# Optimization experiments

Hardware: AMD Instinct MI355X
Metric: run time of the kernel (lower is better)

## Reference

```python
import jax, jax.numpy as jnp
import numpy as np

N_HEAD = 16
MA_K = 0.02          # sigmoid temperature in ma_k_activation
LEAKY_SLOPE = 0.02   # negative_slope in ma_q_activation
NEG_INF = -1e9


def setup_inputs() -> dict:
    key = jax.random.key(0)
    k1, k2, k3, k4 = jax.random.split(key, 4)
    B, T, C = 2, 2048, 1024
    x = jax.random.normal(k1, (B, T, C), dtype=jnp.float32)
    s = 1.0 / np.sqrt(C)
    W_attn = jax.random.normal(k2, (C, 2 * C), dtype=jnp.float32) * s
    W_k2 = jax.random.normal(k3, (C, C), dtype=jnp.float32) * s
    W_proj = jax.random.normal(k4, (C, C), dtype=jnp.float32) * s
    return {"x": x, "W_attn": W_attn, "W_k2": W_k2, "W_proj": W_proj}


def _heads(t, H):
    # [B,T,C] -> [B,H,T,d]
    B, T, C = t.shape
    return t.reshape(B, T, H, C // H).transpose(0, 2, 1, 3)


def reference(x, W_attn, W_k2, W_proj):
    B, T, C = x.shape
    H = N_HEAD
    d = C // H
    scale = 1.0 / jnp.sqrt(jnp.asarray(d, x.dtype))

    qk = x @ W_attn                      # [B,T,2C]
    q, k = jnp.split(qk, 2, axis=-1)
    q = _heads(q, H)                     # [B,H,T,d]
    k = _heads(k, H)
    v = _heads(x, H)                     # v = x

    # --- AR branch: causal softmax attention ---
    scores = jnp.einsum('bhtd,bhsd->bhts', q, k) * scale
    causal = jnp.tril(jnp.ones((T, T), dtype=bool))
    scores = jnp.where(causal, scores, NEG_INF)
    attn = jax.nn.softmax(scores, axis=-1)
    y = jnp.einsum('bhts,bhsd->bhtd', attn, v)   # [B,H,T,d]

    # --- MA branch: causal, softmax-free linear attention on residual ---
    e = v[:, :, 1:, :] - y[:, :, :-1, :]          # [B,H,T-1,d]
    k2 = _heads(x[:, :-1, :] @ W_k2, H)           # [B,H,T-1,d]
    q2 = q[:, :, 1:, :]                           # [B,H,T-1,d]

    qa = -jax.nn.leaky_relu(-q2 * scale, negative_slope=LEAKY_SLOPE)
    ka = jax.nn.sigmoid(MA_K * (k2 * scale))

    w = jnp.einsum('bhtd,bhsd->bhts', qa, ka)     # [B,H,T-1,T-1]
    w = jnp.tril(w)
    y2 = jnp.einsum('bhts,bhsd->bhtd', w, e)      # [B,H,T-1,d]
    y2 = jnp.concatenate([jnp.zeros_like(y2[:, :, :1, :]), y2], axis=2)  # pad front

    def merge(t):  # [B,H,T,d] -> [B,T,C]
        return t.transpose(0, 2, 1, 3).reshape(B, T, C)

    return merge(y) @ W_proj + merge(y2) @ W_proj
```

## Files before the change

### kernel.cpp

```cpp
#include <hip/hip_runtime.h>

typedef unsigned short u16;
typedef u16   u16x4  __attribute__((ext_vector_type(4)));
typedef u16   u16x8  __attribute__((ext_vector_type(8)));
typedef __bf16 bf16x8 __attribute__((ext_vector_type(8)));
typedef float  f32x4  __attribute__((ext_vector_type(4)));

__device__ __forceinline__ float bf2f(u16 v) {
    unsigned u = ((unsigned)v) << 16;
    return __builtin_bit_cast(float, u);
}
__device__ __forceinline__ u16 f2bf(float f) {
    unsigned u = __builtin_bit_cast(unsigned, f);
    u += 0x7fffu + ((u >> 16) & 1u);
    return (u16)(u >> 16);
}

__device__ __forceinline__ size_t kimg_idx(int bh, int s, int d) {
    return ((size_t)(bh * 32 + (s >> 6)) * 4096) + (size_t)(((d >> 3) * 64 + (s & 63)) * 8) + (d & 7);
}
__device__ __forceinline__ size_t vimg_idx(int bh, int s, int d) {
    return ((size_t)(bh * 32 + (s >> 6)) * 4096) + (size_t)((((s & 63) >> 3) * 64 + d) * 8) + (s & 7);
}

__global__ __launch_bounds__(256)
void convert_pack(const float* __restrict__ in, u16* __restrict__ xb,
                  u16* __restrict__ xpack) {
    int i = blockIdx.x * 256 + threadIdx.x;
    int c4 = i & 255, row = i >> 8;
    int s = row & 2047, b = row >> 11;
    float4 v = ((const float4*)in)[i];
    u16x4 o;
    o.x = f2bf(v.x); o.y = f2bf(v.y); o.z = f2bf(v.z); o.w = f2bf(v.w);
    ((u16x4*)xb)[i] = o;
    int h = c4 >> 4, d0 = (c4 & 15) * 4;
    size_t base = vimg_idx(b * 16 + h, s, d0);
    xpack[base]      = o.x;
    xpack[base + 8]  = o.y;
    xpack[base + 16] = o.z;
    xpack[base + 24] = o.w;
}

__global__ __launch_bounds__(256)
void prep_weights(const float* __restrict__ Wa, const float* __restrict__ Wk,
                  const float* __restrict__ Wp, u16* __restrict__ Wta,
                  u16* __restrict__ Wtk, u16* __restrict__ Wtp) {
    __shared__ u16 tile[64][65];
    const int bx = blockIdx.x;
    const float* in; u16* out; int Cd, cx;
    if (bx < 32)      { in = Wa; out = Wta; Cd = 2048; cx = bx; }
    else if (bx < 48) { in = Wk; out = Wtk; Cd = 1024; cx = bx - 32; }
    else              { in = Wp; out = Wtp; Cd = 1024; cx = bx - 48; }
    const int c0 = cx * 64, r0 = blockIdx.y * 64;
    const int tid = threadIdx.x;
#pragma unroll
    for (int i = 0; i < 16; ++i) {
        int idx = tid + i * 256;
        int r = idx >> 6, c = idx & 63;
        tile[r][c] = f2bf(in[(size_t)(r0 + r) * Cd + c0 + c]);
    }
    __syncthreads();
#pragma unroll
    for (int i = 0; i < 16; ++i) {
        int idx = tid + i * 256;
        int r = idx >> 6, c = idx & 63;
        out[(size_t)(c0 + r) * 1024 + r0 + c] = tile[c][r];
    }
}

__global__ __launch_bounds__(256, 3)
void gemm_fused(const u16* __restrict__ A, const u16* __restrict__ Bt,
                u16* __restrict__ qs, u16* __restrict__ kpack,
                u16* __restrict__ kapack) {
    const int K = 1024;
    __shared__ __align__(16) u16 As[4][128][8];
    __shared__ __align__(16) u16 Bs[4][128][8];
    const int tid = threadIdx.x;
    const int wave = tid >> 6, lane = tid & 63;
    const int m0 = blockIdx.y * 128, n0 = blockIdx.x * 128;
    const int wm = (wave >> 1) * 64, wn = (wave & 1) * 64;
    const int q = lane >> 4, mr = lane & 15;
    const int sr = tid >> 2, c8 = tid & 3;
    const int sw = c8 * 2;
    const int rs = q * 2;
    const u16* Ap = A + (size_t)(m0 + sr) * K + c8 * 8;
    const u16* Bp = Bt + (size_t)(n0 + sr) * K + c8 * 8;

    f32x4 acc[4][4];
#pragma unroll
    for (int i = 0; i < 4; ++i)
#pragma unroll
        for (int j = 0; j < 4; ++j) acc[i][j] = f32x4{0.f, 0.f, 0.f, 0.f};

    u16x8 a0, a1, b0, b1;
    auto gload = [&](int k0) {
        a0 = *(const u16x8*)(Ap + k0);
        a1 = *(const u16x8*)(Ap + k0 + (size_t)64 * K);
        b0 = *(const u16x8*)(Bp + k0);
        b1 = *(const u16x8*)(Bp + k0 + (size_t)64 * K);
    };
    gload(0);
    for (int k0 = 0; k0 < K; k0 += 32) {
        __syncthreads();
        *(u16x8*)&As[c8][sr ^ sw][0]        = a0;
        *(u16x8*)&As[c8][(sr + 64) ^ sw][0] = a1;
        *(u16x8*)&Bs[c8][sr ^ sw][0]        = b0;
        *(u16x8*)&Bs[c8][(sr + 64) ^ sw][0] = b1;
        __syncthreads();
        if (k0 + 32 < K) gload(k0 + 32);
        bf16x8 af[4], bfr[4];
#pragma unroll
        for (int i = 0; i < 4; ++i) af[i]  = *(const bf16x8*)&As[q][(wm + i * 16 + mr) ^ rs][0];
#pragma unroll
        for (int j = 0; j < 4; ++j) bfr[j] = *(const bf16x8*)&Bs[q][(wn + j * 16 + mr) ^ rs][0];
#pragma unroll
        for (int i = 0; i < 4; ++i)
#pragma unroll
            for (int j = 0; j < 4; ++j)
                acc[i][j] = __builtin_amdgcn_mfma_f32_16x16x32_bf16(af[i], bfr[j], acc[i][j], 0, 0, 0);
    }
#pragma unroll
    for (int i = 0; i < 4; ++i)
#pragma unroll
        for (int j = 0; j < 4; ++j)
#pragma unroll
            for (int r = 0; r < 4; ++r) {
                int m = m0 + wm + i * 16 + q * 4 + r;
                int n = n0 + wn + j * 16 + mr;
                float v = acc[i][j][r];
                int b = m >> 11, s = m & 2047;
                if (n < 1024) {
                    qs[(size_t)m * 1024 + n] = f2bf(v * 0.125f);
                } else if (n < 2048) {
                    int nn = n - 1024;
                    kpack[kimg_idx(b * 16 + (nn >> 6), s, nn & 63)] = f2bf(v);
                } else {
                    int nn = n - 2048;
                    kapack[kimg_idx(b * 16 + (nn >> 6), s, nn & 63)] =
                        f2bf(1.f / (1.f + __expf(-0.0025f * v)));
                }
            }
}

__global__ __launch_bounds__(256, 2)
void gemm64(const u16* __restrict__ A, const u16* __restrict__ Bt,
            float* __restrict__ Cv, int N, int K) {
    __shared__ __align__(16) u16 As[4][64][8];
    __shared__ __align__(16) u16 Bs[4][128][8];
    const int tid = threadIdx.x;
    const int wave = tid >> 6, lane = tid & 63;
    const int m0 = blockIdx.y * 64, n0 = blockIdx.x * 128;
    const int wn0 = wave * 32;
    const int q = lane >> 4, mr = lane & 15;
    const int sr = tid >> 2, c8 = tid & 3;
    const int sw = c8 * 2, rs = q * 2;
    const u16* Ap = A + (size_t)(m0 + sr) * K + c8 * 8;
    const u16* Bp = Bt + (size_t)(n0 + sr) * K + c8 * 8;

    f32x4 acc[4][2];
#pragma unroll
    for (int i = 0; i < 4; ++i)
#pragma unroll
        for (int j = 0; j < 2; ++j) acc[i][j] = f32x4{0.f, 0.f, 0.f, 0.f};

    u16x8 a0, b0, b1;
    auto gload = [&](int k0) {
        a0 = *(const u16x8*)(Ap + k0);
        b0 = *(const u16x8*)(Bp + k0);
        b1 = *(const u16x8*)(Bp + k0 + (size_t)64 * K);
    };
    gload(0);
    for (int k0 = 0; k0 < K; k0 += 32) {
        __syncthreads();
        if (sr < 64) *(u16x8*)&As[c8][sr ^ sw][0] = a0;
        else         *(u16x8*)&As[c8][(sr - 64) ^ sw][0] = a0;
        *(u16x8*)&Bs[c8][sr ^ sw][0]        = b0;
        *(u16x8*)&Bs[c8][(sr + 64) ^ sw][0] = b1;
        __syncthreads();
        if (k0 + 32 < K) gload(k0 + 32);
        bf16x8 af[4], bfr[2];
#pragma unroll
        for (int i = 0; i < 4; ++i) af[i]  = *(const bf16x8*)&As[q][(i * 16 + mr) ^ rs][0];
#pragma unroll
        for (int j = 0; j < 2; ++j) bfr[j] = *(const bf16x8*)&Bs[q][(wn0 + j * 16 + mr) ^ rs][0];
#pragma unroll
        for (int i = 0; i < 4; ++i)
#pragma unroll
            for (int j = 0; j < 2; ++j)
                acc[i][j] = __builtin_amdgcn_mfma_f32_16x16x32_bf16(af[i], bfr[j], acc[i][j], 0, 0, 0);
    }
#pragma unroll
    for (int i = 0; i < 4; ++i)
#pragma unroll
        for (int j = 0; j < 2; ++j)
#pragma unroll
            for (int r = 0; r < 4; ++r) {
                int m = m0 + i * 16 + q * 4 + r;
                int n = n0 + wn0 + j * 16 + mr;
                Cv[(size_t)m * N + n] = acc[i][j][r];
            }
}

__global__ __launch_bounds__(256, 2)
void flash_mfma(const u16* __restrict__ qs, const u16* __restrict__ kpack,
                const u16* __restrict__ xpack, u16* __restrict__ Opart,
                float* __restrict__ lpart) {
    __shared__ __align__(16) u16 Ks[8][64][8];
    __shared__ __align__(16) u16 Vs[8][64][8];
    __shared__ __align__(16) u16 Ps[4][16][72];
    const int bh = blockIdx.y, b = bh >> 4, hc = (bh & 15) * 64;
    const int z = blockIdx.z;
    const int tid = threadIdx.x, w = tid >> 6, lane = tid & 63;
    const int n16 = lane & 15, quad = lane >> 4;
    const u16* kbase = kpack + (size_t)bh * 32 * 4096;
    const u16* vbase = xpack + (size_t)bh * 32 * 4096;
    u16* Ob = Opart + (size_t)z * 4096 * 1024;
    float* lb = lpart + z * 65536;

    for (int rep = 0; rep < 2; ++rep) {
        const int T = rep ? 15 - (int)blockIdx.x : (int)blockIdx.x;
        const int t0 = T * 128;
        const int nchunk = 2 * T + 2;

        bf16x8 qf[2][2];
#pragma unroll
        for (int mt = 0; mt < 2; ++mt) {
            const int trow = t0 + (w + mt * 4) * 16 + n16;
            const u16* qp = &qs[(size_t)(b * 2048 + trow) * 1024 + hc + quad * 8];
            qf[mt][0] = *(const bf16x8*)qp;
            qf[mt][1] = *(const bf16x8*)(qp + 32);
        }

        f32x4 O[2][4];
        float lsum[2][4];
#pragma unroll
        for (int mt = 0; mt < 2; ++mt)
#pragma unroll
            for (int jt = 0; jt < 4; ++jt) { O[mt][jt] = f32x4{0.f, 0.f, 0.f, 0.f}; }
#pragma unroll
        for (int mt = 0; mt < 2; ++mt)
#pragma unroll
            for (int r = 0; r < 4; ++r) lsum[mt][r] = 0.f;

        u16x8 kr0, kr1, vr0, vr1;
        auto pref = [&](int c) {
            const u16* kc = kbase + (size_t)c * 4096;
            const u16* vc = vbase + (size_t)c * 4096;
            kr0 = *(const u16x8*)(kc + tid * 8);
            kr1 = *(const u16x8*)(kc + (256 + tid) * 8);
            vr0 = *(const u16x8*)(vc + tid * 8);
            vr1 = *(const u16x8*)(vc + (256 + tid) * 8);
        };
        if (z < nchunk) pref(z);

        for (int c = z; c < nchunk; c += 2) {
            __syncthreads();
            *(u16x8*)((u16*)Ks + tid * 8)         = kr0;
            *(u16x8*)((u16*)Ks + (256 + tid) * 8) = kr1;
            *(u16x8*)((u16*)Vs + tid * 8)         = vr0;
            *(u16x8*)((u16*)Vs + (256 + tid) * 8) = vr1;
            __syncthreads();
            if (c + 2 < nchunk) pref(c + 2);

            f32x4 S[2][4];
#pragma unroll
            for (int mt = 0; mt < 2; ++mt)
#pragma unroll
                for (int jt = 0; jt < 4; ++jt) S[mt][jt] = f32x4{0.f, 0.f, 0.f, 0.f};
#pragma unroll
            for (int ks = 0; ks < 2; ++ks)
#pragma unroll
                for (int jt = 0; jt < 4; ++jt) {
                    bf16x8 kf = *(const bf16x8*)&Ks[ks * 4 + quad][jt * 16 + n16][0];
                    S[0][jt] = __builtin_amdgcn_mfma_f32_16x16x32_bf16(qf[0][ks], kf, S[0][jt], 0, 0, 0);
                    S[1][jt] = __builtin_amdgcn_mfma_f32_16x16x32_bf16(qf[1][ks], kf, S[1][jt], 0, 0, 0);
                }
            bf16x8 vf[2][4];
#pragma unroll
            for (int ks = 0; ks < 2; ++ks)
#pragma unroll
                for (int jt = 0; jt < 4; ++jt)
                    vf[ks][jt] = *(const bf16x8*)&Vs[ks * 4 + quad][jt * 16 + n16][0];

#pragma unroll
            for (int mt = 0; mt < 2; ++mt) {
                if (mt == 0 && c == 2 * T + 1) continue;
                float p[4][4];
#pragma unroll
                for (int reg = 0; reg < 4; ++reg)
#pragma unroll
                    for (int jt = 0; jt < 4; ++jt)
                        p[reg][jt] = __expf(S[mt][jt][reg]);
                if (c == 2 * T + mt) {
#pragma unroll
                    for (int reg = 0; reg < 4; ++reg) {
                        const int tr = t0 + (w + mt * 4) * 16 + quad * 4 + reg;
#pragma unroll
                        for (int jt = 0; jt < 4; ++jt)
                            if (c * 64 + jt * 16 + n16 > tr) p[reg][jt] = 0.f;
                    }
                }
#pragma unroll
                for (int reg = 0; reg < 4; ++reg) {
                    lsum[mt][reg] += (p[reg][0] + p[reg][1]) + (p[reg][2] + p[reg][3]);
#pragma unroll
                    for (int jt = 0; jt < 4; ++jt)
                        Ps[w][quad * 4 + reg][jt * 16 + n16] = f2bf(p[reg][jt]);
                }
                bf16x8 pf[2];
#pragma unroll
                for (int ks = 0; ks < 2; ++ks)
                    pf[ks] = *(const bf16x8*)&Ps[w][n16][ks * 32 + quad * 8];
#pragma unroll
                for (int ks = 0; ks < 2; ++ks)
#pragma unroll
                    for (int jt = 0; jt < 4; ++jt)
                        O[mt][jt] = __builtin_amdgcn_mfma_f32_16x16x32_bf16(pf[ks], vf[ks][jt], O[mt][jt], 0, 0, 0);
            }
        }

#pragma unroll
        for (int mt = 0; mt < 2; ++mt)
#pragma unroll
            for (int reg = 0; reg < 4; ++reg) {
                float l = lsum[mt][reg];
#pragma unroll
                for (int off = 1; off < 16; off <<= 1) l += __shfl_xor(l, off, 64);
                const int tr = t0 + (w + mt * 4) * 16 + quad * 4 + reg;
                if (n16 == 0) lb[bh * 2048 + tr] = l;
                const size_t row = (size_t)(b * 2048 + tr) * 1024 + hc;
#pragma unroll
                for (int jt = 0; jt < 4; ++jt)
                    Ob[row + jt * 16 + n16] = f2bf(O[mt][jt][reg]);
            }
    }
}

__global__ __launch_bounds__(256)
void combine_flash(const u16* __restrict__ Opart, const float* __restrict__ lpart,
                   const u16* __restrict__ xb, u16* __restrict__ y,
                   u16* __restrict__ epack) {
    int i = blockIdx.x * 256 + threadIdx.x;
    int c4 = i & 255, row = i >> 8, t = row & 2047, b = row >> 11;
    int h = c4 >> 4, d0 = (c4 & 15) * 4;
    size_t off = (size_t)row * 1024 + c4 * 4;
    u16x4 o0 = *(const u16x4*)&Opart[off];
    u16x4 o1 = *(const u16x4*)&Opart[(size_t)4096 * 1024 + off];
    int lrow = (b * 16 + h) * 2048 + t;
    float inv = 1.f / (lpart[lrow] + lpart[65536 + lrow]);
    float y0 = (bf2f(o0.x) + bf2f(o1.x)) * inv;
    float y1 = (bf2f(o0.y) + bf2f(o1.y)) * inv;
    float y2 = (bf2f(o0.z) + bf2f(o1.z)) * inv;
    float y3 = (bf2f(o0.w) + bf2f(o1.w)) * inv;
    u16x4 yo;
    yo.x = f2bf(y0); yo.y = f2bf(y1); yo.z = f2bf(y2); yo.w = f2bf(y3);
    *(u16x4*)&y[off] = yo;
    float e0 = 0.f, e1 = 0.f, e2 = 0.f, e3 = 0.f;
    if (t < 2047) {
        u16x4 xv = *(const u16x4*)&xb[off + 1024];
        e0 = bf2f(xv.x) - y0; e1 = bf2f(xv.y) - y1;
        e2 = bf2f(xv.z) - y2; e3 = bf2f(xv.w) - y3;
    }
    size_t base = vimg_idx(b * 16 + h, t, d0);
    epack[base]      = f2bf(e0);
    epack[base + 8]  = f2bf(e1);
    epack[base + 16] = f2bf(e2);
    epack[base + 24] = f2bf(e3);
}

__global__ __launch_bounds__(256, 2)
void arma_mfma(const u16* __restrict__ qs, const u16* __restrict__ kapack,
               const u16* __restrict__ epack, u16* __restrict__ Opart) {
    __shared__ __align__(16) u16 Ks[8][64][8];
    __shared__ __align__(16) u16 Es[8][64][8];
    __shared__ __align__(16) u16 Ps[4][16][72];
    const int bh = blockIdx.y, b = bh >> 4, hc = (bh & 15) * 64;
    const int z = blockIdx.z;
    const int tid = threadIdx.x, w = tid >> 6, lane = tid & 63;
    const int n16 = lane & 15, quad = lane >> 4;
    const u16* kbase = kapack + (size_t)bh * 32 * 4096;
    const u16* vbase = epack + (size_t)bh * 32 * 4096;
    u16* Ob = Opart + (size_t)z * 4096 * 1024;

    for (int rep = 0; rep < 2; ++rep) {
        const int T = rep ? 15 - (int)blockIdx.x : (int)blockIdx.x;
        const int t0 = T * 128;
        const int nchunk = 2 * T + 2;

        bf16x8 qf[2][2];
#pragma unroll
        for (int mt = 0; mt < 2; ++mt) {
            const int trow = t0 + (w + mt * 4) * 16 + n16;
            const u16* qp = &qs[(size_t)(b * 2048 + trow) * 1024 + hc + quad * 8];
#pragma unroll
            for (int ks = 0; ks < 2; ++ks) {
                u16x8 qv = *(const u16x8*)(qp + ks * 32);
                u16x8 o;
#pragma unroll
                for (int j = 0; j < 8; ++j) {
                    float zv = bf2f(qv[j]);
                    o[j] = f2bf(zv < 0.f ? zv : 0.02f * zv);
                }
                qf[mt][ks] = __builtin_bit_cast(bf16x8, o);
            }
        }

        f32x4 O[2][4];
#pragma unroll
        for (int mt = 0; mt < 2; ++mt)
#pragma unroll
            for (int jt = 0; jt < 4; ++jt) O[mt][jt] = f32x4{0.f, 0.f, 0.f, 0.f};

        u16x8 kr0, kr1, vr0, vr1;
        auto pref = [&](int c) {
            const u16* kc = kbase + (size_t)c * 4096;
            const u16* vc = vbase + (size_t)c * 4096;
            kr0 = *(const u16x8*)(kc + tid * 8);
            kr1 = *(const u16x8*)(kc + (256 + tid) * 8);
            vr0 = *(const u16x8*)(vc + tid * 8);
            vr1 = *(const u16x8*)(vc + (256 + tid) * 8);
        };
        if (z < nchunk) pref(z);

        for (int c = z; c < nchunk; c += 2) {
            __syncthreads();
            *(u16x8*)((u16*)Ks + tid * 8)         = kr0;
            *(u16x8*)((u16*)Ks + (256 + tid) * 8) = kr1;
            *(u16x8*)((u16*)Es + tid * 8)         = vr0;
            *(u16x8*)((u16*)Es + (256 + tid) * 8) = vr1;
            __syncthreads();
            if (c + 2 < nchunk) pref(c + 2);

            f32x4 S[2][4];
#pragma unroll
            for (int mt = 0; mt < 2; ++mt)
#pragma unroll
                for (int jt = 0; jt < 4; ++jt) S[mt][jt] = f32x4{0.f, 0.f, 0.f, 0.f};
#pragma unroll
            for (int ks = 0; ks < 2; ++ks)
#pragma unroll
                for (int jt = 0; jt < 4; ++jt) {
                    bf16x8 kf = *(const bf16x8*)&Ks[ks * 4 + quad][jt * 16 + n16][0];
                    S[0][jt] = __builtin_amdgcn_mfma_f32_16x16x32_bf16(qf[0][ks], kf, S[0][jt], 0, 0, 0);
                    S[1][jt] = __builtin_amdgcn_mfma_f32_16x16x32_bf16(qf[1][ks], kf, S[1][jt], 0, 0, 0);
                }
            bf16x8 vf[2][4];
#pragma unroll
            for (int ks = 0; ks < 2; ++ks)
#pragma unroll
                for (int jt = 0; jt < 4; ++jt)
                    vf[ks][jt] = *(const bf16x8*)&Es[ks * 4 + quad][jt * 16 + n16][0];

#pragma unroll
            for (int mt = 0; mt < 2; ++mt) {
                if (mt == 0 && c == 2 * T + 1) continue;
                if (c == 2 * T + mt) {
#pragma unroll
                    for (int reg = 0; reg < 4; ++reg) {
                        const int tr = t0 + (w + mt * 4) * 16 + quad * 4 + reg;
#pragma unroll
                        for (int jt = 0; jt < 4; ++jt)
                            if (c * 64 + jt * 16 + n16 >= tr) S[mt][jt][reg] = 0.f;
                    }
                }
#pragma unroll
                for (int reg = 0; reg < 4; ++reg)
#pragma unroll
                    for (int jt = 0; jt < 4; ++jt)
                        Ps[w][quad * 4 + reg][jt * 16 + n16] = f2bf(S[mt][jt][reg]);
                bf16x8 pf[2];
#pragma unroll
                for (int ks = 0; ks < 2; ++ks)
                    pf[ks] = *(const bf16x8*)&Ps[w][n16][ks * 32 + quad * 8];
#pragma unroll
                for (int ks = 0; ks < 2; ++ks)
#pragma unroll
                    for (int jt = 0; jt < 4; ++jt)
                        O[mt][jt] = __builtin_amdgcn_mfma_f32_16x16x32_bf16(pf[ks], vf[ks][jt], O[mt][jt], 0, 0, 0);
            }
        }

#pragma unroll
        for (int mt = 0; mt < 2; ++mt)
#pragma unroll
            for (int reg = 0; reg < 4; ++reg) {
                const int tr = t0 + (w + mt * 4) * 16 + quad * 4 + reg;
                const size_t row = (size_t)(b * 2048 + tr) * 1024 + hc;
#pragma unroll
                for (int jt = 0; jt < 4; ++jt)
                    Ob[row + jt * 16 + n16] = f2bf(O[mt][jt][reg]);
            }
    }
}

__global__ __launch_bounds__(256)
void combine_arma(const u16* __restrict__ Opart, const u16* __restrict__ y,
                  u16* __restrict__ ys) {
    int i = blockIdx.x * 256 + threadIdx.x;
    size_t off = (size_t)i * 4;
    u16x4 o0 = *(const u16x4*)&Opart[off];
    u16x4 o1 = *(const u16x4*)&Opart[(size_t)4096 * 1024 + off];
    u16x4 yv = *(const u16x4*)&y[off];
    u16x4 r;
    r.x = f2bf(bf2f(yv.x) + bf2f(o0.x) + bf2f(o1.x));
    r.y = f2bf(bf2f(yv.y) + bf2f(o0.y) + bf2f(o1.y));
    r.z = f2bf(bf2f(yv.z) + bf2f(o0.z) + bf2f(o1.z));
    r.w = f2bf(bf2f(yv.w) + bf2f(o0.w) + bf2f(o1.w));
    *(u16x4*)&ys[off] = r;
}

extern "C" void kernel_launch(void* const* d_in, const int* in_sizes, int n_in,
                              void* d_out, int out_size, void* d_ws, size_t ws_size,
                              hipStream_t stream) {
    const float* x      = (const float*)d_in[0];
    const float* W_attn = (const float*)d_in[1];
    const float* W_k2   = (const float*)d_in[2];
    const float* W_proj = (const float*)d_in[3];
    float* out = (float*)d_out;

    char* w = (char*)d_ws;
    u16* xb      = (u16*)w; w += (size_t)4096 * 1024 * 2;
    u16* Wt_attn = (u16*)w; w += (size_t)2048 * 1024 * 2;
    u16* Wt_k2   = (u16*)w; w += (size_t)1024 * 1024 * 2;
    u16* Wt_proj = (u16*)w; w += (size_t)1024 * 1024 * 2;
    u16* qs      = (u16*)w; w += (size_t)4096 * 1024 * 2;
    u16* kpack   = (u16*)w; w += (size_t)4096 * 1024 * 2;
    u16* kapack  = (u16*)w; w += (size_t)4096 * 1024 * 2;
    u16* xpack   = (u16*)w; w += (size_t)4096 * 1024 * 2;
    u16* y       = (u16*)w; w += (size_t)4096 * 1024 * 2;
    u16* epack   = (u16*)w; w += (size_t)4096 * 1024 * 2;
    u16* Opart   = (u16*)w; w += (size_t)2 * 4096 * 1024 * 2;
    float* lpart = (float*)w; w += (size_t)2 * 65536 * 4;
    u16* ys = xb;

    convert_pack<<<dim3(4096), dim3(256), 0, stream>>>(x, xb, xpack);
    prep_weights<<<dim3(64, 16), dim3(256), 0, stream>>>(W_attn, W_k2, W_proj,
                                                         Wt_attn, Wt_k2, Wt_proj);
    gemm_fused<<<dim3(24, 32), dim3(256), 0, stream>>>(xb, Wt_attn, qs, kpack, kapack);
    flash_mfma<<<dim3(8, 32, 2), dim3(256), 0, stream>>>(qs, kpack, xpack, Opart, lpart);
    combine_flash<<<dim3(4096), dim3(256), 0, stream>>>(Opart, lpart, xb, y, epack);
    arma_mfma<<<dim3(8, 32, 2), dim3(256), 0, stream>>>(qs, kapack, epack, Opart);
    combine_arma<<<dim3(4096), dim3(256), 0, stream>>>(Opart, y, ys);
    gemm64<<<dim3(8, 64), dim3(256), 0, stream>>>(ys, Wt_proj, out, 1024, 1024);
}
```

Baseline: 260.8 us.

## Stage GEMM tiles via direct global-to-LDS async loads instead of register staging

Both GEMM kernels now copy A/B tiles straight into shared memory with global_load_lds 16-byte transfers, replacing the register-staged software prefetch and the XOR swizzle. This cuts VGPR use and the separate LDS store instructions. In exchange, the next tile is no longer prefetched during compute: each iteration waits on vmcnt(0) before the barrier, which exposes global load latency. The unswizzled LDS layout may also bring back bank conflicts on the fragment reads.

Result: slower. 296.6 us (+13.7%).

```diff
diff --git a/kernel.cpp b/kernel.cpp
--- a/kernel.cpp
+++ b/kernel.cpp
@@ -14,6 +14,13 @@
     unsigned u = __builtin_bit_cast(unsigned, f);
     u += 0x7fffu + ((u >> 16) & 1u);
     return (u16)(u >> 16);
+}
+
+__device__ __forceinline__ void async16(const u16* g, u16* l) {
+    __builtin_amdgcn_global_load_lds(
+        (const __attribute__((address_space(1))) unsigned int*)g,
+        (__attribute__((address_space(3))) unsigned int*)l,
+        16, 0, 0);
 }
 
 __device__ __forceinline__ size_t kimg_idx(int bh, int s, int d) {
@@ -80,11 +87,16 @@
     const int m0 = blockIdx.y * 128, n0 = blockIdx.x * 128;
     const int wm = (wave >> 1) * 64, wn = (wave & 1) * 64;
     const int q = lane >> 4, mr = lane & 15;
-    const int sr = tid >> 2, c8 = tid & 3;
-    const int sw = c8 * 2;
-    const int rs = q * 2;
-    const u16* Ap = A + (size_t)(m0 + sr) * K + c8 * 8;
-    const u16* Bp = Bt + (size_t)(n0 + sr) * K + c8 * 8;
+
+    const int s0 = tid, s1 = 256 + tid;
+    const u16* gA0 = A  + (size_t)(m0 + (s0 & 127)) * K + (s0 >> 7) * 8;
+    const u16* gA1 = A  + (size_t)(m0 + (s1 & 127)) * K + (s1 >> 7) * 8;
+    const u16* gB0 = Bt + (size_t)(n0 + (s0 & 127)) * K + (s0 >> 7) * 8;
+    const u16* gB1 = Bt + (size_t)(n0 + (s1 & 127)) * K + (s1 >> 7) * 8;
+    u16* lA0 = &As[0][0][0] + (size_t)s0 * 8;
+    u16* lA1 = &As[0][0][0] + (size_t)s1 * 8;
+    u16* lB0 = &Bs[0][0][0] + (size_t)s0 * 8;
+    u16* lB1 = &Bs[0][0][0] + (size_t)s1 * 8;
 
     f32x4 acc[4][4];
 #pragma unroll
@@ -92,27 +104,19 @@
 #pragma unroll
         for (int j = 0; j < 4; ++j) acc[i][j] = f32x4{0.f, 0.f, 0.f, 0.f};
 
-    u16x8 a0, a1, b0, b1;
-    auto gload = [&](int k0) {
-        a0 = *(const u16x8*)(Ap + k0);
-        a1 = *(const u16x8*)(Ap + k0 + (size_t)64 * K);
-        b0 = *(const u16x8*)(Bp + k0);
-        b1 = *(const u16x8*)(Bp + k0 + (size_t)64 * K);
-    };
-    gload(0);
     for (int k0 = 0; k0 < K; k0 += 32) {
         __syncthreads();
-        *(u16x8*)&As[c8][sr ^ sw][0]        = a0;
-        *(u16x8*)&As[c8][(sr + 64) ^ sw][0] = a1;
-        *(u16x8*)&Bs[c8][sr ^ sw][0]        = b0;
-        *(u16x8*)&Bs[c8][(sr + 64) ^ sw][0] = b1;
+        async16(gA0 + k0, lA0);
+        async16(gA1 + k0, lA1);
+        async16(gB0 + k0, lB0);
+        async16(gB1 + k0, lB1);
+        asm volatile("s_waitcnt vmcnt(0)" ::: "memory");
         __syncthreads();
-        if (k0 + 32 < K) gload(k0 + 32);
         bf16x8 af[4], bfr[4];
 #pragma unroll
-        for (int i = 0; i < 4; ++i) af[i]  = *(const bf16x8*)&As[q][(wm + i * 16 + mr) ^ rs][0];
-#pragma unroll
-        for (int j = 0; j < 4; ++j) bfr[j] = *(const bf16x8*)&Bs[q][(wn + j * 16 + mr) ^ rs][0];
+        for (int i = 0; i < 4; ++i) af[i]  = *(const bf16x8*)&As[q][wm + i * 16 + mr][0];
+#pragma unroll
+        for (int j = 0; j < 4; ++j) bfr[j] = *(const bf16x8*)&Bs[q][wn + j * 16 + mr][0];
 #pragma unroll
         for (int i = 0; i < 4; ++i)
 #pragma unroll
@@ -152,10 +156,14 @@
     const int m0 = blockIdx.y * 64, n0 = blockIdx.x * 128;
     const int wn0 = wave * 32;
     const int q = lane >> 4, mr = lane & 15;
-    const int sr = tid >> 2, c8 = tid & 3;
-    const int sw = c8 * 2, rs = q * 2;
-    const u16* Ap = A + (size_t)(m0 + sr) * K + c8 * 8;
-    const u16* Bp = Bt + (size_t)(n0 + sr) * K + c8 * 8;
+
+    const u16* gA = A + (size_t)(m0 + (tid & 63)) * K + (tid >> 6) * 8;
+    u16* lA = &As[0][0][0] + (size_t)tid * 8;
+    const int s1 = 256 + tid;
+    const u16* gB0 = Bt + (size_t)(n0 + (tid & 127)) * K + (tid >> 7) * 8;
+    const u16* gB1 = Bt + (size_t)(n0 + (s1 & 127)) * K + (s1 >> 7) * 8;
+    u16* lB0 = &Bs[0][0][0] + (size_t)tid * 8;
+    u16* lB1 = &Bs[0][0][0] + (size_t)s1 * 8;
 
     f32x4 acc[4][2];
 #pragma unroll
@@ -163,26 +171,18 @@
 #pragma unroll
         for (int j = 0; j < 2; ++j) acc[i][j] = f32x4{0.f, 0.f, 0.f, 0.f};
 
-    u16x8 a0, b0, b1;
-    auto gload = [&](int k0) {
-        a0 = *(const u16x8*)(Ap + k0);
-        b0 = *(const u16x8*)(Bp + k0);
-        b1 = *(const u16x8*)(Bp + k0 + (size_t)64 * K);
-    };
-    gload(0);
     for (int k0 = 0; k0 < K; k0 += 32) {
         __syncthreads();
-        if (sr < 64) *(u16x8*)&As[c8][sr ^ sw][0] = a0;
-        else         *(u16x8*)&As[c8][(sr - 64) ^ sw][0] = a0;
-        *(u16x8*)&Bs[c8][sr ^ sw][0]        = b0;
-        *(u16x8*)&Bs[c8][(sr + 64) ^ sw][0] = b1;
+        async16(gA + k0, lA);
+        async16(gB0 + k0, lB0);
+        async16(gB1 + k0, lB1);
+        asm volatile("s_waitcnt vmcnt(0)" ::: "memory");
         __syncthreads();
-        if (k0 + 32 < K) gload(k0 + 32);
         bf16x8 af[4], bfr[2];
 #pragma unroll
-        for (int i = 0; i < 4; ++i) af[i]  = *(const bf16x8*)&As[q][(i * 16 + mr) ^ rs][0];
-#pragma unroll
-        for (int j = 0; j < 2; ++j) bfr[j] = *(const bf16x8*)&Bs[q][(wn0 + j * 16 + mr) ^ rs][0];
+        for (int i = 0; i < 4; ++i) af[i]  = *(const bf16x8*)&As[q][i * 16 + mr][0];
+#pragma unroll
+        for (int j = 0; j < 2; ++j) bfr[j] = *(const bf16x8*)&Bs[q][wn0 + j * 16 + mr][0];
 #pragma unroll
         for (int i = 0; i < 4; ++i)
 #pragma unroll
```
